# Kernel optimization log

Measured on AMD Instinct MI355X. Metric: run time of the kernel, lower is better.

Reference implementation:

```python
import jax, jax.numpy as jnp
import numpy as np

D_MODEL, D_K, D_V = 1024, 64, 64
B, S = 4, 4096


def setup_inputs() -> dict:
    key = jax.random.key(0)
    ks = jax.random.split(key, 13)
    s = 1.0 / np.sqrt(D_MODEL)
    inp = {
        "q": jax.random.normal(ks[0], (B, S, D_MODEL), jnp.float32),
        "k": jax.random.normal(ks[1], (B, S, D_MODEL), jnp.float32),
        "v": jax.random.normal(ks[2], (B, S, D_MODEL), jnp.float32),
        "mask": jax.random.randint(ks[3], (1, S, S), 0, 2, jnp.int32),
        "Wq": jax.random.normal(ks[4], (D_K, D_MODEL), jnp.float32) * s,
        "bq": jax.random.normal(ks[5], (D_K,), jnp.float32) * s,
        "Wk": jax.random.normal(ks[6], (D_K, D_MODEL), jnp.float32) * s,
        "bk": jax.random.normal(ks[7], (D_K,), jnp.float32) * s,
        "Wv": jax.random.normal(ks[8], (D_V, D_MODEL), jnp.float32) * s,
        "bv": jax.random.normal(ks[9], (D_V,), jnp.float32) * s,
        "Wo": jax.random.normal(ks[10], (D_MODEL, D_V), jnp.float32) / np.sqrt(D_V),
        "bo": jax.random.normal(ks[11], (D_MODEL,), jnp.float32) / np.sqrt(D_V),
    }
    return inp


def reference(q, k, v, mask, Wq, bq, Wk, bk, Wv, bv, Wo, bo):
    # linear projections (torch Linear: x @ W.T + b)
    qh = jnp.einsum("bsd,kd->bsk", q, Wq) + bq   # [B,S,d_k]
    kh = jnp.einsum("bsd,kd->bsk", k, Wk) + bk   # [B,S,d_k]
    vh = jnp.einsum("bsd,vd->bsv", v, Wv) + bv   # [B,S,d_v]
    scale = 1.0 / jnp.sqrt(jnp.float32(D_K))
    scores = jnp.einsum("bqk,bmk->bqm", qh, kh) * scale  # [B,S,S]
    scores = jnp.where(mask == 0, jnp.float32(-1e9), scores)
    attn = jax.nn.softmax(scores, axis=-1)
    out = jnp.einsum("bqm,bmv->bqv", attn, vh)   # [B,S,d_v]
    return jnp.einsum("bqv,dv->bqd", out, Wo) + bo
```

## Files before the change

kernel.cpp:

```cpp
#include <hip/hip_runtime.h>
#include <cmath>

typedef __attribute__((ext_vector_type(8))) short bf16x8;
typedef __attribute__((ext_vector_type(4))) short bf16x4;
typedef __attribute__((ext_vector_type(4))) float f32x4;

constexpr int B_ = 4;
constexpr int S_ = 4096;
constexpr int DM_ = 1024;
constexpr int DK_ = 64;
constexpr int NROW = B_ * S_;

__device__ __forceinline__ short f2bf(float x) {
  union { float f; unsigned u; } c; c.f = x;
  unsigned r = (c.u + 0x7FFF + ((c.u >> 16) & 1)) >> 16;
  return (short)r;
}
__device__ __forceinline__ float bf2f(short h) {
  union { float f; unsigned u; } c; c.u = ((unsigned)(unsigned short)h) << 16;
  return c.f;
}

__global__ __launch_bounds__(256) void maskpack(
    const int* __restrict__ mask, unsigned long long* __restrict__ bits) {
  const int wid = (blockIdx.x * 256 + threadIdx.x) >> 6;
  const int lane = threadIdx.x & 63;
  const size_t base = (size_t)wid * 4096;
  for (int it = 0; it < 64; ++it) {
    int m = mask[base + it * 64 + lane];
    unsigned long long b = __ballot(m != 0);
    if (lane == 0) bits[(size_t)wid * 64 + it] = b;
  }
}

__global__ __launch_bounds__(256) void proj_mfma(
    const float* __restrict__ q, const float* __restrict__ k,
    const float* __restrict__ v,
    const float* __restrict__ Wq, const float* __restrict__ bq,
    const float* __restrict__ Wk, const float* __restrict__ bk,
    const float* __restrict__ Wv, const float* __restrict__ bv,
    short* __restrict__ qh, short* __restrict__ kh, short* __restrict__ vhT) {
  const int mat = blockIdx.z;
  const float* X    = mat == 0 ? q  : (mat == 1 ? k  : v);
  const float* W    = mat == 0 ? Wq : (mat == 1 ? Wk : Wv);
  const float* bias = mat == 0 ? bq : (mat == 1 ? bk : bv);

  __shared__ float Xs[128][36];
  __shared__ short Ws[64][40];

  const int t = threadIdx.x;
  const int row0 = blockIdx.x * 128;
  const int lane = t & 63, w = t >> 6, quad = lane >> 4, l16 = lane & 15;

  f32x4 acc[2][4] = {};

  for (int k0 = 0; k0 < DM_; k0 += 32) {
    __syncthreads();
    {
      int r = t >> 1, off = (t & 1) * 16;
      const float* src = X + (size_t)(row0 + r) * DM_ + k0 + off;
#pragma unroll
      for (int i = 0; i < 4; ++i)
        *(f32x4*)&Xs[r][off + 4 * i] = *(const f32x4*)(src + 4 * i);
    }
    {
      int c = t >> 2, kk = (t & 3) * 8;
      const float* src = W + (size_t)c * DM_ + k0 + kk;
      f32x4 b0 = *(const f32x4*)src;
      f32x4 b1 = *(const f32x4*)(src + 4);
      bf16x8 wb;
#pragma unroll
      for (int j = 0; j < 4; ++j) { wb[j] = f2bf(b0[j]); wb[j + 4] = f2bf(b1[j]); }
      *(bf16x8*)&Ws[c][kk] = wb;
    }
    __syncthreads();

    bf16x8 bw[4];
#pragma unroll
    for (int ct = 0; ct < 4; ++ct)
      bw[ct] = *(const bf16x8*)&Ws[16 * ct + l16][quad * 8];

#pragma unroll
    for (int rt = 0; rt < 2; ++rt) {
      const float* xp = &Xs[32 * w + 16 * rt + l16][quad * 8];
      f32x4 x0 = *(const f32x4*)xp;
      f32x4 x1 = *(const f32x4*)(xp + 4);
      bf16x8 ahi, alo;
#pragma unroll
      for (int j = 0; j < 4; ++j) {
        short h0 = f2bf(x0[j]); ahi[j] = h0;     alo[j]     = f2bf(x0[j] - bf2f(h0));
        short h1 = f2bf(x1[j]); ahi[j + 4] = h1; alo[j + 4] = f2bf(x1[j] - bf2f(h1));
      }
#pragma unroll
      for (int ct = 0; ct < 4; ++ct) {
        acc[rt][ct] = __builtin_amdgcn_mfma_f32_16x16x32_bf16(ahi, bw[ct], acc[rt][ct], 0, 0, 0);
        acc[rt][ct] = __builtin_amdgcn_mfma_f32_16x16x32_bf16(alo, bw[ct], acc[rt][ct], 0, 0, 0);
      }
    }
  }

  float bs[4];
#pragma unroll
  for (int ct = 0; ct < 4; ++ct) bs[ct] = bias[16 * ct + l16];

  short* dstq = (mat == 0) ? qh : kh;
#pragma unroll
  for (int rt = 0; rt < 2; ++rt)
#pragma unroll
    for (int ct = 0; ct < 4; ++ct)
#pragma unroll
      for (int reg = 0; reg < 4; ++reg) {
        int r = row0 + 32 * w + 16 * rt + quad * 4 + reg;
        int c = 16 * ct + l16;
        short hv = f2bf(acc[rt][ct][reg] + bs[ct]);
        if (mat == 2)
          vhT[((size_t)(r >> 12) * DK_ + c) * S_ + (r & 4095)] = hv;
        else
          dstq[(size_t)r * DK_ + c] = hv;
      }
}

__global__ __launch_bounds__(256) void attn_mfma(
    const short* __restrict__ qh, const short* __restrict__ kh,
    const short* __restrict__ vhT, const unsigned int* __restrict__ mbits,
    float* __restrict__ o_ws) {
  __shared__ short ks[64][72];
  __shared__ short vt[64][72];
  __shared__ short ps[4][16][72];

  const int b = blockIdx.y;
  const int q0 = blockIdx.x * 64;
  const int t = threadIdx.x, lane = t & 63, w = t >> 6;
  const int quad = lane >> 4, l16 = lane & 15;
  const int myq = q0 + 16 * w + l16;

  bf16x8 qf[2];
  {
    const short* src = qh + ((size_t)b * S_ + myq) * DK_ + quad * 8;
    qf[0] = *(const bf16x8*)src;
    qf[1] = *(const bf16x8*)(src + 32);
  }

  f32x4 ao[4] = {};
  float m_i = -INFINITY, l_i = 0.0f;

  const int sr = t >> 2;
  const int sseg = t & 3;

  for (int kt = 0; kt < S_; kt += 64) {
    __syncthreads();
    {
      const short* srck = kh + ((size_t)b * S_ + kt + sr) * DK_;
      *(bf16x8*)&ks[sr][8 * sseg]       = *(const bf16x8*)(srck + 8 * sseg);
      *(bf16x8*)&ks[sr][8 * (sseg + 4)] = *(const bf16x8*)(srck + 8 * (sseg + 4));
      const short* srcv = vhT + ((size_t)b * DK_ + sr) * S_ + kt;
      *(bf16x8*)&vt[sr][8 * sseg]       = *(const bf16x8*)(srcv + 8 * sseg);
      *(bf16x8*)&vt[sr][8 * (sseg + 4)] = *(const bf16x8*)(srcv + 8 * (sseg + 4));
    }
    const uint2 mw = *(const uint2*)&mbits[(size_t)myq * 128 + (kt >> 5)];
    __syncthreads();

    f32x4 sacc[4] = {};
#pragma unroll
    for (int c = 0; c < 2; ++c)
#pragma unroll
      for (int tt = 0; tt < 4; ++tt) {
        bf16x8 a = *(const bf16x8*)&ks[16 * tt + l16][c * 32 + quad * 8];
        sacc[tt] = __builtin_amdgcn_mfma_f32_16x16x32_bf16(a, qf[c], sacc[tt], 0, 0, 0);
      }

    float sc[16];
#pragma unroll
    for (int tt = 0; tt < 4; ++tt) {
      unsigned wrd = (tt & 2) ? mw.y : mw.x;
      int base = (tt & 1) * 16 + quad * 4;
#pragma unroll
      for (int r = 0; r < 4; ++r)
        sc[tt * 4 + r] = ((wrd >> (base + r)) & 1) ? sacc[tt][r] * 0.125f : -1e9f;
    }

    float mx = sc[0];
#pragma unroll
    for (int i = 1; i < 16; ++i) mx = fmaxf(mx, sc[i]);
    mx = fmaxf(mx, __shfl_xor(mx, 16));
    mx = fmaxf(mx, __shfl_xor(mx, 32));
    float m_new = fmaxf(m_i, mx);
    float alpha = __expf(m_i - m_new);
    float p[16], sum = 0.0f;
#pragma unroll
    for (int i = 0; i < 16; ++i) { p[i] = __expf(sc[i] - m_new); sum += p[i]; }
    sum += __shfl_xor(sum, 16);
    sum += __shfl_xor(sum, 32);
    l_i = l_i * alpha + sum;
    m_i = m_new;

#pragma unroll
    for (int tt = 0; tt < 4; ++tt) {
      bf16x4 pk;
#pragma unroll
      for (int r = 0; r < 4; ++r) pk[r] = f2bf(p[tt * 4 + r]);
      *(bf16x4*)&ps[w][l16][16 * tt + quad * 4] = pk;
    }

#pragma unroll
    for (int dt = 0; dt < 4; ++dt)
#pragma unroll
      for (int r = 0; r < 4; ++r) ao[dt][r] *= alpha;

#pragma unroll
    for (int c = 0; c < 2; ++c) {
      bf16x8 bp = *(const bf16x8*)&ps[w][l16][c * 32 + quad * 8];
#pragma unroll
      for (int dt = 0; dt < 4; ++dt) {
        bf16x8 av = *(const bf16x8*)&vt[16 * dt + l16][c * 32 + quad * 8];
        ao[dt] = __builtin_amdgcn_mfma_f32_16x16x32_bf16(av, bp, ao[dt], 0, 0, 0);
      }
    }
  }

  const float inv = 1.0f / l_i;
#pragma unroll
  for (int dt = 0; dt < 4; ++dt) {
    f32x4 o;
#pragma unroll
    for (int r = 0; r < 4; ++r) o[r] = ao[dt][r] * inv;
    *(f32x4*)&o_ws[((size_t)b * S_ + myq) * DK_ + 16 * dt + quad * 4] = o;
  }
}

__global__ __launch_bounds__(256) void outproj_mfma(
    const float* __restrict__ o_in, const float* __restrict__ Wo,
    const float* __restrict__ bo, float* __restrict__ out) {
  __shared__ short os[64][72];
  __shared__ short wos[256][72];

  const int t = threadIdx.x, lane = t & 63, w = t >> 6;
  const int quad = lane >> 4, l16 = lane & 15;
  const int s0 = blockIdx.y * 64;
  const int dm0 = blockIdx.x * 256;

  {
    int r = t >> 2, cq = (t & 3) * 16;
    const float* src = o_in + (size_t)(s0 + r) * DK_ + cq;
    f32x4 a0 = *(const f32x4*)src, a1 = *(const f32x4*)(src + 4);
    f32x4 a2 = *(const f32x4*)(src + 8), a3 = *(const f32x4*)(src + 12);
    bf16x8 v0, v1;
#pragma unroll
    for (int j = 0; j < 4; ++j) {
      v0[j] = f2bf(a0[j]); v0[j + 4] = f2bf(a1[j]);
      v1[j] = f2bf(a2[j]); v1[j + 4] = f2bf(a3[j]);
    }
    *(bf16x8*)&os[r][cq] = v0;
    *(bf16x8*)&os[r][cq + 8] = v1;
  }
#pragma unroll
  for (int pass = 0; pass < 4; ++pass) {
    int r = pass * 64 + (t >> 2), cq = (t & 3) * 16;
    const float* src = Wo + (size_t)(dm0 + r) * DK_ + cq;
    f32x4 a0 = *(const f32x4*)src, a1 = *(const f32x4*)(src + 4);
    f32x4 a2 = *(const f32x4*)(src + 8), a3 = *(const f32x4*)(src + 12);
    bf16x8 v0, v1;
#pragma unroll
    for (int j = 0; j < 4; ++j) {
      v0[j] = f2bf(a0[j]); v0[j + 4] = f2bf(a1[j]);
      v1[j] = f2bf(a2[j]); v1[j + 4] = f2bf(a3[j]);
    }
    *(bf16x8*)&wos[r][cq] = v0;
    *(bf16x8*)&wos[r][cq + 8] = v1;
  }
  __syncthreads();

  bf16x8 af[2];
#pragma unroll
  for (int c = 0; c < 2; ++c)
    af[c] = *(const bf16x8*)&os[16 * w + l16][c * 32 + quad * 8];

  f32x4 acc[16] = {};
#pragma unroll
  for (int c = 0; c < 2; ++c)
#pragma unroll
    for (int nt = 0; nt < 16; ++nt) {
      bf16x8 bw = *(const bf16x8*)&wos[16 * nt + l16][c * 32 + quad * 8];
      acc[nt] = __builtin_amdgcn_mfma_f32_16x16x32_bf16(af[c], bw, acc[nt], 0, 0, 0);
    }

  float bias_r[16];
#pragma unroll
  for (int nt = 0; nt < 16; ++nt) bias_r[nt] = bo[dm0 + 16 * nt + l16];

#pragma unroll
  for (int nt = 0; nt < 16; ++nt)
#pragma unroll
    for (int reg = 0; reg < 4; ++reg) {
      int s = s0 + 16 * w + quad * 4 + reg;
      int dm = dm0 + 16 * nt + l16;
      out[(size_t)s * DM_ + dm] = acc[nt][reg] + bias_r[nt];
    }
}

extern "C" void kernel_launch(void* const* d_in, const int* in_sizes, int n_in,
                              void* d_out, int out_size, void* d_ws,
                              size_t ws_size, hipStream_t stream) {
  (void)in_sizes; (void)n_in; (void)out_size; (void)ws_size;
  const float* q  = (const float*)d_in[0];
  const float* k  = (const float*)d_in[1];
  const float* v  = (const float*)d_in[2];
  const int* mask = (const int*)d_in[3];
  const float* Wq = (const float*)d_in[4];
  const float* bq = (const float*)d_in[5];
  const float* Wk = (const float*)d_in[6];
  const float* bk = (const float*)d_in[7];
  const float* Wv = (const float*)d_in[8];
  const float* bv = (const float*)d_in[9];
  const float* Wo = (const float*)d_in[10];
  const float* bo = (const float*)d_in[11];
  float* out = (float*)d_out;

  short* qh = (short*)d_ws;
  short* kh = qh + (size_t)NROW * DK_;
  short* vhT = kh + (size_t)NROW * DK_;
  unsigned int* mbits = (unsigned int*)(vhT + (size_t)NROW * DK_);
  float* o_ws = (float*)(mbits + (size_t)S_ * 128);

  maskpack<<<1024, 256, 0, stream>>>(mask, (unsigned long long*)mbits);
  proj_mfma<<<dim3(NROW / 128, 1, 3), 256, 0, stream>>>(
      q, k, v, Wq, bq, Wk, bk, Wv, bv, qh, kh, vhT);
  attn_mfma<<<dim3(S_ / 64, B_), 256, 0, stream>>>(qh, kh, vhT, mbits, o_ws);
  outproj_mfma<<<dim3(DM_ / 256, NROW / 64), 256, 0, stream>>>(o_ws, Wo, bo, out);
}
```

Before: 457.9 us.

## Split attention over key ranges with combine pass and deepen projection K-tile

Attention now splits the key sequence into up to four chunks across a new grid dimension, writing unnormalized partial outputs plus per-row max and sum, then a new combine kernel merges them and emits bf16 output for the output projection. This raises the attention grid from 256 blocks to as many as 1024 so more compute units stay busy. The projection kernel now stages 64 columns of K per iteration instead of 32, halving the number of barriers. The cost is extra workspace traffic for the partials and one more kernel launch, and the split count depends on how large the workspace is.

```diff
diff --git a/kernel.cpp b/kernel.cpp
--- a/kernel.cpp
+++ b/kernel.cpp
@@ -45,8 +45,8 @@
   const float* W    = mat == 0 ? Wq : (mat == 1 ? Wk : Wv);
   const float* bias = mat == 0 ? bq : (mat == 1 ? bk : bv);
 
-  __shared__ float Xs[128][36];
-  __shared__ short Ws[64][40];
+  __shared__ float Xs[128][68];
+  __shared__ short Ws[64][72];
 
   const int t = threadIdx.x;
   const int row0 = blockIdx.x * 128;
@@ -54,47 +54,56 @@
 
   f32x4 acc[2][4] = {};
 
-  for (int k0 = 0; k0 < DM_; k0 += 32) {
+  for (int k0 = 0; k0 < DM_; k0 += 64) {
     __syncthreads();
     {
-      int r = t >> 1, off = (t & 1) * 16;
-      const float* src = X + (size_t)(row0 + r) * DM_ + k0 + off;
-#pragma unroll
-      for (int i = 0; i < 4; ++i)
-        *(f32x4*)&Xs[r][off + 4 * i] = *(const f32x4*)(src + 4 * i);
+      const int rr = t >> 3, cc = (t & 7) * 8;
+#pragma unroll
+      for (int pass = 0; pass < 4; ++pass) {
+        int r = pass * 32 + rr;
+        const float* src = X + (size_t)(row0 + r) * DM_ + k0 + cc;
+        *(f32x4*)&Xs[r][cc]     = *(const f32x4*)src;
+        *(f32x4*)&Xs[r][cc + 4] = *(const f32x4*)(src + 4);
+      }
     }
     {
-      int c = t >> 2, kk = (t & 3) * 8;
+      int c = t >> 2, kk = (t & 3) * 16;
       const float* src = W + (size_t)c * DM_ + k0 + kk;
-      f32x4 b0 = *(const f32x4*)src;
-      f32x4 b1 = *(const f32x4*)(src + 4);
-      bf16x8 wb;
-#pragma unroll
-      for (int j = 0; j < 4; ++j) { wb[j] = f2bf(b0[j]); wb[j + 4] = f2bf(b1[j]); }
-      *(bf16x8*)&Ws[c][kk] = wb;
+      f32x4 a0 = *(const f32x4*)src, a1 = *(const f32x4*)(src + 4);
+      f32x4 a2 = *(const f32x4*)(src + 8), a3 = *(const f32x4*)(src + 12);
+      bf16x8 w0, w1;
+#pragma unroll
+      for (int j = 0; j < 4; ++j) {
+        w0[j] = f2bf(a0[j]); w0[j + 4] = f2bf(a1[j]);
+        w1[j] = f2bf(a2[j]); w1[j + 4] = f2bf(a3[j]);
+      }
+      *(bf16x8*)&Ws[c][kk]     = w0;
+      *(bf16x8*)&Ws[c][kk + 8] = w1;
     }
     __syncthreads();
 
-    bf16x8 bw[4];
-#pragma unroll
-    for (int ct = 0; ct < 4; ++ct)
-      bw[ct] = *(const bf16x8*)&Ws[16 * ct + l16][quad * 8];
-
-#pragma unroll
-    for (int rt = 0; rt < 2; ++rt) {
-      const float* xp = &Xs[32 * w + 16 * rt + l16][quad * 8];
-      f32x4 x0 = *(const f32x4*)xp;
-      f32x4 x1 = *(const f32x4*)(xp + 4);
-      bf16x8 ahi, alo;
-#pragma unroll
-      for (int j = 0; j < 4; ++j) {
-        short h0 = f2bf(x0[j]); ahi[j] = h0;     alo[j]     = f2bf(x0[j] - bf2f(h0));
-        short h1 = f2bf(x1[j]); ahi[j + 4] = h1; alo[j + 4] = f2bf(x1[j] - bf2f(h1));
-      }
-#pragma unroll
-      for (int ct = 0; ct < 4; ++ct) {
-        acc[rt][ct] = __builtin_amdgcn_mfma_f32_16x16x32_bf16(ahi, bw[ct], acc[rt][ct], 0, 0, 0);
-        acc[rt][ct] = __builtin_amdgcn_mfma_f32_16x16x32_bf16(alo, bw[ct], acc[rt][ct], 0, 0, 0);
+#pragma unroll
+    for (int c = 0; c < 2; ++c) {
+      bf16x8 bw[4];
+#pragma unroll
+      for (int ct = 0; ct < 4; ++ct)
+        bw[ct] = *(const bf16x8*)&Ws[16 * ct + l16][c * 32 + quad * 8];
+#pragma unroll
+      for (int rt = 0; rt < 2; ++rt) {
+        const float* xp = &Xs[32 * w + 16 * rt + l16][c * 32 + quad * 8];
+        f32x4 x0 = *(const f32x4*)xp;
+        f32x4 x1 = *(const f32x4*)(xp + 4);
+        bf16x8 ahi, alo;
+#pragma unroll
+        for (int j = 0; j < 4; ++j) {
+          short h0 = f2bf(x0[j]); ahi[j] = h0;     alo[j]     = f2bf(x0[j] - bf2f(h0));
+          short h1 = f2bf(x1[j]); ahi[j + 4] = h1; alo[j + 4] = f2bf(x1[j] - bf2f(h1));
+        }
+#pragma unroll
+        for (int ct = 0; ct < 4; ++ct) {
+          acc[rt][ct] = __builtin_amdgcn_mfma_f32_16x16x32_bf16(ahi, bw[ct], acc[rt][ct], 0, 0, 0);
+          acc[rt][ct] = __builtin_amdgcn_mfma_f32_16x16x32_bf16(alo, bw[ct], acc[rt][ct], 0, 0, 0);
+        }
       }
     }
   }
@@ -123,16 +132,21 @@
 __global__ __launch_bounds__(256) void attn_mfma(
     const short* __restrict__ qh, const short* __restrict__ kh,
     const short* __restrict__ vhT, const unsigned int* __restrict__ mbits,
-    float* __restrict__ o_ws) {
+    float* __restrict__ Opart, float* __restrict__ mpart,
+    float* __restrict__ lpart, int ns) {
   __shared__ short ks[64][72];
   __shared__ short vt[64][72];
   __shared__ short ps[4][16][72];
 
-  const int b = blockIdx.y;
+  const int b = blockIdx.z;
+  const int split = blockIdx.y;
   const int q0 = blockIdx.x * 64;
   const int t = threadIdx.x, lane = t & 63, w = t >> 6;
   const int quad = lane >> 4, l16 = lane & 15;
   const int myq = q0 + 16 * w + l16;
+
+  const int kt0 = split * (S_ / ns);
+  const int kt1 = kt0 + S_ / ns;
 
   bf16x8 qf[2];
   {
@@ -147,7 +161,7 @@
   const int sr = t >> 2;
   const int sseg = t & 3;
 
-  for (int kt = 0; kt < S_; kt += 64) {
+  for (int kt = kt0; kt < kt1; kt += 64) {
     __syncthreads();
     {
       const short* srck = kh + ((size_t)b * S_ + kt + sr) * DK_;
@@ -218,18 +232,53 @@
     }
   }
 
-  const float inv = 1.0f / l_i;
-#pragma unroll
-  for (int dt = 0; dt < 4; ++dt) {
-    f32x4 o;
-#pragma unroll
-    for (int r = 0; r < 4; ++r) o[r] = ao[dt][r] * inv;
-    *(f32x4*)&o_ws[((size_t)b * S_ + myq) * DK_ + 16 * dt + quad * 4] = o;
-  }
+  const size_t prow = (size_t)split * NROW + (size_t)b * S_ + myq;
+#pragma unroll
+  for (int dt = 0; dt < 4; ++dt)
+    *(f32x4*)&Opart[prow * DK_ + 16 * dt + quad * 4] = ao[dt];
+  if (quad == 0) {
+    mpart[prow] = m_i;
+    lpart[prow] = l_i;
+  }
+}
+
+__global__ __launch_bounds__(256) void attn_combine(
+    const float* __restrict__ Opart, const float* __restrict__ mpart,
+    const float* __restrict__ lpart, short* __restrict__ o_bf, int ns) {
+  const int t = threadIdx.x;
+  const int row = blockIdx.x * 64 + (t >> 2);
+  const int c0 = (t & 3) * 16;
+
+  float M = -INFINITY;
+  for (int s = 0; s < ns; ++s) M = fmaxf(M, mpart[(size_t)s * NROW + row]);
+  float L = 0.0f, wt[4];
+  for (int s = 0; s < ns; ++s) {
+    wt[s] = __expf(mpart[(size_t)s * NROW + row] - M);
+    L += wt[s] * lpart[(size_t)s * NROW + row];
+  }
+  float acc[16] = {};
+  for (int s = 0; s < ns; ++s) {
+    const float* src = Opart + ((size_t)s * NROW + row) * DK_ + c0;
+#pragma unroll
+    for (int j = 0; j < 16; j += 4) {
+      f32x4 vv = *(const f32x4*)(src + j);
+#pragma unroll
+      for (int r = 0; r < 4; ++r) acc[j + r] += wt[s] * vv[r];
+    }
+  }
+  const float inv = 1.0f / L;
+  bf16x8 o0, o1;
+#pragma unroll
+  for (int j = 0; j < 8; ++j) {
+    o0[j] = f2bf(acc[j] * inv);
+    o1[j] = f2bf(acc[j + 8] * inv);
+  }
+  *(bf16x8*)&o_bf[(size_t)row * DK_ + c0]     = o0;
+  *(bf16x8*)&o_bf[(size_t)row * DK_ + c0 + 8] = o1;
 }
 
 __global__ __launch_bounds__(256) void outproj_mfma(
-    const float* __restrict__ o_in, const float* __restrict__ Wo,
+    const short* __restrict__ o_bf, const float* __restrict__ Wo,
     const float* __restrict__ bo, float* __restrict__ out) {
   __shared__ short os[64][72];
   __shared__ short wos[256][72];
@@ -241,17 +290,9 @@
 
   {
     int r = t >> 2, cq = (t & 3) * 16;
-    const float* src = o_in + (size_t)(s0 + r) * DK_ + cq;
-    f32x4 a0 = *(const f32x4*)src, a1 = *(const f32x4*)(src + 4);
-    f32x4 a2 = *(const f32x4*)(src + 8), a3 = *(const f32x4*)(src + 12);
-    bf16x8 v0, v1;
-#pragma unroll
-    for (int j = 0; j < 4; ++j) {
-      v0[j] = f2bf(a0[j]); v0[j + 4] = f2bf(a1[j]);
-      v1[j] = f2bf(a2[j]); v1[j + 4] = f2bf(a3[j]);
-    }
-    *(bf16x8*)&os[r][cq] = v0;
-    *(bf16x8*)&os[r][cq + 8] = v1;
+    const short* src = o_bf + (size_t)(s0 + r) * DK_ + cq;
+    *(bf16x8*)&os[r][cq]     = *(const bf16x8*)src;
+    *(bf16x8*)&os[r][cq + 8] = *(const bf16x8*)(src + 8);
   }
 #pragma unroll
   for (int pass = 0; pass < 4; ++pass) {
@@ -265,7 +306,7 @@
       v0[j] = f2bf(a0[j]); v0[j + 4] = f2bf(a1[j]);
       v1[j] = f2bf(a2[j]); v1[j + 4] = f2bf(a3[j]);
     }
-    *(bf16x8*)&wos[r][cq] = v0;
+    *(bf16x8*)&wos[r][cq]     = v0;
     *(bf16x8*)&wos[r][cq + 8] = v1;
   }
   __syncthreads();
@@ -301,7 +342,7 @@
 extern "C" void kernel_launch(void* const* d_in, const int* in_sizes, int n_in,
                               void* d_out, int out_size, void* d_ws,
                               size_t ws_size, hipStream_t stream) {
-  (void)in_sizes; (void)n_in; (void)out_size; (void)ws_size;
+  (void)in_sizes; (void)n_in; (void)out_size;
   const float* q  = (const float*)d_in[0];
   const float* k  = (const float*)d_in[1];
   const float* v  = (const float*)d_in[2];
@@ -316,15 +357,26 @@
   const float* bo = (const float*)d_in[11];
   float* out = (float*)d_out;
 
-  short* qh = (short*)d_ws;
-  short* kh = qh + (size_t)NROW * DK_;
+  short* qh  = (short*)d_ws;
+  short* kh  = qh + (size_t)NROW * DK_;
   short* vhT = kh + (size_t)NROW * DK_;
   unsigned int* mbits = (unsigned int*)(vhT + (size_t)NROW * DK_);
-  float* o_ws = (float*)(mbits + (size_t)S_ * 128);
+  short* o_bf = (short*)(mbits + (size_t)S_ * 128);
+  float* mpart = (float*)(o_bf + (size_t)NROW * DK_);
+  float* lpart = mpart + 4 * NROW;
+  float* Opart = lpart + 4 * NROW;
+
+  const size_t base_bytes = (size_t)((char*)Opart - (char*)d_ws);
+  const size_t per_split = (size_t)NROW * DK_ * sizeof(float);
+  int ns = 1;
+  if (ws_size >= base_bytes + 4 * per_split) ns = 4;
+  else if (ws_size >= base_bytes + 2 * per_split) ns = 2;
 
   maskpack<<<1024, 256, 0, stream>>>(mask, (unsigned long long*)mbits);
   proj_mfma<<<dim3(NROW / 128, 1, 3), 256, 0, stream>>>(
       q, k, v, Wq, bq, Wk, bk, Wv, bv, qh, kh, vhT);
-  attn_mfma<<<dim3(S_ / 64, B_), 256, 0, stream>>>(qh, kh, vhT, mbits, o_ws);
-  outproj_mfma<<<dim3(DM_ / 256, NROW / 64), 256, 0, stream>>>(o_ws, Wo, bo, out);
-}
+  attn_mfma<<<dim3(S_ / 64, ns, B_), 256, 0, stream>>>(
+      qh, kh, vhT, mbits, Opart, mpart, lpart, ns);
+  attn_combine<<<NROW / 64, 256, 0, stream>>>(Opart, mpart, lpart, o_bf, ns);
+  outproj_mfma<<<dim3(DM_ / 256, NROW / 64), 256, 0, stream>>>(o_bf, Wo, bo, out);
+}
```

Result: faster. 387.6 us (-15.3%).
